# Optimization experiments

Measured on AMD Instinct MI355X. Metric: run time of the kernel, lower is better.

Reference implementation:

```python
import jax, jax.numpy as jnp
import numpy as np
from jax.scipy.special import logsumexp

N = 16    # taxa
K = 128   # particles
S = 512   # sites (batch == full sites)
A = 4     # alphabet (DNA)
D = 64    # embedding dim
C = 16    # site-position encoding dim
PRIOR_BL = 1.0
RATE = 1.0 / PRIOR_BL


def _log_double_factorials(n_max):
    v = np.zeros(n_max + 1)
    for i in range(2, n_max + 1):
        v[i] = v[i - 2] + np.log(i)
    return jnp.asarray(v, dtype=jnp.float32)

LOG_DF = _log_double_factorials(2 * N)


def _gather_K(arr, idx):
    return arr[jnp.arange(arr.shape[0]), idx]


def _remove2(arr_t, i1, i2):
    # drop entries i1, i2 along leading axis, preserving order (static output size t-2)
    t = arr_t.shape[0]
    ar = jnp.arange(t)
    keep = (ar != i1) & (ar != i2)
    order = jnp.argsort(~keep)[: t - 2]  # stable sort: kept entries first, in order
    return arr_t[order]


def _merge_K(arr, i1, i2, new_K):
    # replace_with_merged_K: remove the two merged subtrees, append the new one
    removed = jax.vmap(_remove2)(arr, i1, i2)
    return jnp.concatenate([removed, new_K[:, None]], axis=1)


def _stat_probs(emb_VxD, siteC_SxC, W_stat, W_site):
    logits = (emb_VxD @ W_stat)[:, None, :] + (siteC_SxC @ W_site)[None]  # V,S,A
    return jax.nn.softmax(logits, axis=-1)


def _log_P_F81(stat_KxSxA, b_K):
    # F81 rate matrix Q = pi - I  =>  P(t) = e^{-t} I + (1 - e^{-t}) pi (closed-form expm)
    e = jnp.exp(-b_K)[:, None, None, None]
    P = e * jnp.eye(A, dtype=stat_KxSxA.dtype) + (1.0 - e) * stat_KxSxA[:, :, None, :]
    return jnp.log(P + 1e-30)  # K,S,A,A


def _fel_half(logP, log_fel):
    # logsumexp_b ( logP[k,s,a,b] + log_fel[k,s,b] )
    return logsumexp(logP + log_fel[:, :, None, :], axis=-1)


def _forward(data_NxSxA, data_batched_NxSxA, site_positions_SxSfull, W_enc, W_merge, W_stat, W_pos, W_site):
    key = jax.random.key(42)
    siteC = site_positions_SxSfull @ W_pos                      # S,C
    emb0 = jnp.tanh(data_NxSxA.reshape(N, -1) @ W_enc)          # N,D (seq_encoder)
    embeddings = jnp.broadcast_to(emb0[None], (K, N, D))
    log_fel = jnp.broadcast_to(jnp.log(data_batched_NxSxA)[None], (K, N, S, A))
    leaf_counts = jnp.ones((K, N), jnp.int32)
    merge1 = jnp.zeros((K, 0), jnp.int32)
    merge2 = jnp.zeros((K, 0), jnp.int32)
    br1 = jnp.zeros((K, 0), dtype=data_NxSxA.dtype)
    br2 = jnp.zeros((K, 0), dtype=data_NxSxA.dtype)
    log_pi = jnp.zeros(K)
    log_w = jnp.zeros(K)
    log_lik = jnp.zeros(K)
    log_ws = []
    log_rate = jnp.log(jnp.asarray(RATE, data_NxSxA.dtype))
    for r in range(N - 1):
        t = N - r
        key, k1, k2, k3, k4 = jax.random.split(key, 5)
        # ---- categorical resampling ----
        idxK = jax.random.categorical(k1, log_w, shape=(K,))
        merge1, merge2 = merge1[idxK], merge2[idxK]
        br1, br2 = br1[idxK], br2[idxK]
        leaf_counts = leaf_counts[idxK]
        embeddings = embeddings[idxK]
        log_fel = log_fel[idxK]
        log_pi, log_w = log_pi[idxK], log_w[idxK]
        # ---- proposal: uniform pair + exponential branch lengths ----
        i1s, i2s = np.triu_indices(t, 1)
        npairs = len(i1s)
        p = jax.random.randint(k2, (K,), 0, npairs)
        idx1 = jnp.asarray(i1s, jnp.int32)[p]
        idx2 = jnp.asarray(i2s, jnp.int32)[p]
        b1 = jax.random.exponential(k3, (K,)) * PRIOR_BL
        b2 = jax.random.exponential(k4, (K,)) * PRIOR_BL
        log_v_plus = -jnp.log(float(npairs)) + (log_rate - RATE * b1) + (log_rate - RATE * b2)
        log_v_minus = jnp.zeros(K)
        e1, e2 = _gather_K(embeddings, idx1), _gather_K(embeddings, idx2)
        new_emb = jnp.tanh(jnp.concatenate([e1, e2], axis=-1) @ W_merge)  # K,D
        # ---- record merge history (concat_K) ----
        merge1 = jnp.concatenate([merge1, idx1[:, None]], axis=1)
        merge2 = jnp.concatenate([merge2, idx2[:, None]], axis=1)
        br1 = jnp.concatenate([br1, b1[:, None]], axis=1)
        br2 = jnp.concatenate([br2, b2[:, None]], axis=1)
        new_lc = _gather_K(leaf_counts, idx1) + _gather_K(leaf_counts, idx2)
        f1, f2 = _gather_K(log_fel, idx1), _gather_K(log_fel, idx2)
        leaf_counts = _merge_K(leaf_counts, idx1, idx2, new_lc)
        embeddings = _merge_K(embeddings, idx1, idx2, new_emb)
        # ---- Felsenstein pruning step at the new internal node ----
        stat_new = _stat_probs(new_emb, siteC, W_stat, W_site)  # K,S,A
        new_fel = _fel_half(_log_P_F81(stat_new, b1), f1) + _fel_half(_log_P_F81(stat_new, b2), f2)
        log_fel = _merge_K(log_fel, idx1, idx2, new_fel)
        # ---- forest log-likelihood and log pi ----
        tn = t - 1
        stat_all = _stat_probs(embeddings.reshape(K * tn, D), siteC, W_stat, W_site)
        log_stat = jnp.log(stat_all).reshape(K, tn, S, A)
        log_lik = jnp.sum(logsumexp(log_fel + log_stat, axis=-1), axis=(1, 2))  # K
        log_top = -jnp.sum(LOG_DF[jnp.clip(2 * leaf_counts - 3, 0)], axis=1)
        log_branch = jnp.sum(log_rate - RATE * br1, axis=1) + jnp.sum(log_rate - RATE * br2, axis=1)
        prev_log_pi = log_pi
        log_pi = log_lik + log_top + log_branch
        log_w = log_pi - prev_log_pi + log_v_minus - log_v_plus
        log_ws.append(log_w)
    log_ws = jnp.stack(log_ws)  # (N-1), K
    log_Z_SMC = jnp.sum(logsumexp(log_ws - jnp.log(float(K)), axis=1))
    best = jnp.argmax(log_lik)
    return (log_Z_SMC, log_lik, merge1[best], merge2[best], br1[best], br2[best])


def setup_inputs() -> dict:
    key = jax.random.key(0)
    ks = jax.random.split(key, 6)
    data = jax.random.uniform(ks[0], (N, S, A), minval=0.05, maxval=1.0)
    return {
        "data_NxSxA": data,
        "data_batched_NxSxA": data,
        "site_positions_SxSfull": jnp.eye(S, dtype=jnp.float32),
        "W_enc": jax.random.normal(ks[1], (S * A, D)) / float(np.sqrt(S * A)),
        "W_merge": jax.random.normal(ks[2], (2 * D, D)) / float(np.sqrt(2 * D)),
        "W_stat": jax.random.normal(ks[3], (D, A)) / float(np.sqrt(D)),
        "W_pos": jax.random.normal(ks[4], (S, C)) / float(np.sqrt(S)),
        "W_site": jax.random.normal(ks[5], (C, A)) / float(np.sqrt(C)),
    }


def reference(data_NxSxA, data_batched_NxSxA, site_positions_SxSfull, W_enc, W_merge, W_stat, W_pos, W_site):
    return _forward(data_NxSxA, data_batched_NxSxA, site_positions_SxSfull, W_enc, W_merge, W_stat, W_pos, W_site)
```

## Files before the change

kernel.cpp:

```cpp
#include <hip/hip_runtime.h>
#include <stdint.h>


#define NN 16
#define KK 128
#define SS 512
#define NR 15
#define PARTITIONABLE 1
#define TINYF 1.17549435e-38f
#define NROWS (NN + NR * KK)

__host__ __device__ __forceinline__ void tf2x32(uint32_t k0, uint32_t k1,
                                                uint32_t c0, uint32_t c1,
                                                uint32_t* o0, uint32_t* o1) {
  uint32_t ks2 = k0 ^ k1 ^ 0x1BD11BDAu;
  uint32_t x0 = c0 + k0, x1 = c1 + k1;
  uint32_t ks[3] = {k0, k1, ks2};
  const uint32_t RA[4] = {13u, 15u, 26u, 6u};
  const uint32_t RB[4] = {17u, 29u, 16u, 24u};
#pragma unroll
  for (int i = 0; i < 5; ++i) {
#pragma unroll
    for (int j = 0; j < 4; ++j) {
      uint32_t r = (i & 1) ? RB[j] : RA[j];
      x0 += x1;
      x1 = (x1 << r) | (x1 >> (32u - r));
      x1 ^= x0;
    }
    x0 += ks[(i + 1) % 3];
    x1 += ks[(i + 2) % 3] + (uint32_t)(i + 1);
  }
  *o0 = x0; *o1 = x1;
}

__device__ __forceinline__ uint32_t rbits32(uint32_t ka, uint32_t kb,
                                            uint32_t i, uint32_t total) {
#if PARTITIONABLE
  uint32_t o0, o1;
  tf2x32(ka, kb, 0u, i, &o0, &o1);
  return o0 ^ o1;
#else
  uint32_t half = total >> 1;
  uint32_t o0, o1;
  if (i < half) { tf2x32(ka, kb, i, i + half, &o0, &o1); return o0; }
  tf2x32(ka, kb, i - half, i, &o0, &o1);
  return o1;
#endif
}

__device__ __forceinline__ float bits_unif(uint32_t b) {
  return __uint_as_float((b >> 9) | 0x3f800000u) - 1.0f;
}

__device__ __forceinline__ float xla_tanh(float x) {
  float ax = fabsf(x);
  float xc = fminf(fmaxf(x, -7.90531110763549805f), 7.90531110763549805f);
  float x2 = __fmul_rn(xc, xc);
  float num = -2.76076847742355e-16f;
  num = __fadd_rn(__fmul_rn(x2, num), 2.00018790482477e-13f);
  num = __fadd_rn(__fmul_rn(x2, num), -8.60467152213735e-11f);
  num = __fadd_rn(__fmul_rn(x2, num), 5.12229709037114e-08f);
  num = __fadd_rn(__fmul_rn(x2, num), 1.48572235717979e-05f);
  num = __fadd_rn(__fmul_rn(x2, num), 6.37261928875436e-04f);
  num = __fadd_rn(__fmul_rn(x2, num), 4.89352455891786e-03f);
  num = __fmul_rn(xc, num);
  float den = 1.19825839466702e-06f;
  den = __fadd_rn(__fmul_rn(x2, den), 1.18534705686654e-04f);
  den = __fadd_rn(__fmul_rn(x2, den), 2.26843463243900e-03f);
  den = __fadd_rn(__fmul_rn(x2, den), 4.89352518554385e-03f);
  float r = __fdiv_rn(num, den);
  return (ax < 0.0004f) ? x : r;
}

__device__ __forceinline__ float fin_or0(float v) {
  return (v > -INFINITY && v < INFINITY) ? v : 0.0f;
}

__device__ __forceinline__ void fold8(float& ll, const float4* b4, int n4) {
  if (n4 <= 0) return;
  float4 pre[8];
#pragma unroll
  for (int i = 0; i < 8; ++i) pre[i] = b4[i];
  for (int q = 8; q <= n4; q += 8) {
    float4 cur[8];
#pragma unroll
    for (int i = 0; i < 8; ++i) cur[i] = pre[i];
    if (q < n4) {
#pragma unroll
      for (int i = 0; i < 8; ++i) pre[i] = b4[q + i];
    }
#pragma unroll
    for (int i = 0; i < 8; ++i) {
      ll = __fadd_rn(ll, cur[i].x);
      ll = __fadd_rn(ll, cur[i].y);
      ll = __fadd_rn(ll, cur[i].z);
      ll = __fadd_rn(ll, cur[i].w);
    }
  }
}

__global__ void k_setup(const float* datab, const float* Wpos, const float* Wsite,
                        float* fel_pool, float* sitelog, float* logw0,
                        float* logpi0, int* lc_pool, int* ilist0, float* logdf) {
  int b = blockIdx.x, tid = threadIdx.x;
  if (b < 64) {
    int id = b * 256 + tid;
    fel_pool[id] = logf(datab[id]);
    fel_pool[16384 + id] = logf(datab[16384 + id]);
  } else if (b < 72) {
    int id = (b - 64) * 256 + tid;
    int s = id >> 2, aa = id & 3;
    float acc = 0.0f;
    for (int c = 0; c < 16; ++c) acc = fmaf(Wpos[s * 16 + c], Wsite[c * 4 + aa], acc);
    sitelog[id] = acc;
  } else {
    if (tid < KK) {
      logw0[tid] = 0.0f;
      logpi0[tid] = 0.0f;
      for (int nn2 = 0; nn2 < NN; ++nn2) ilist0[tid * 16 + nn2] = nn2;
    }
    if (tid < NN) lc_pool[tid] = 1;
    if (tid == 0) {
      double vv[33];
      vv[0] = 0.0; vv[1] = 0.0;
      for (int i = 2; i <= 32; ++i) vv[i] = vv[i - 2] + log((double)i);
      for (int i = 0; i < 33; ++i) logdf[i] = (float)vv[i];
    }
  }
}

__global__ __launch_bounds__(64) void k_emb0(const float* data, const float* Wenc,
                                             const float* Wstat, float* emb_pool,
                                             float* ew0) {
  int n = blockIdx.x, d = threadIdx.x;
  __shared__ float ne[64];
  const float* dp = data + n * 2048;
  const float* wp = Wenc + d;
  float acc = 0.0f;
#pragma unroll 32
  for (int i = 0; i < 2048; ++i) acc = fmaf(dp[i], wp[(size_t)i * 64], acc);
  float v = xla_tanh(acc);
  ne[d] = v;
  emb_pool[n * 64 + d] = v;
  __syncthreads();
  if (d < 4) {
    float s = 0.0f;
    for (int c = 0; c < 64; ++c) s = fmaf(ne[c], Wstat[c * 4 + d], s);
    ew0[n * 4 + d] = s;
  }
}

__global__ void k_leafterm(const float* fel_pool, const float* ew0,
                           const float* sitelog, float* st_pool) {
  int id = blockIdx.x * blockDim.x + threadIdx.x;
  if (id >= NN * SS) return;
  int n = id >> 9, s = id & 511;
  float lg[4], ex[4], stat[4];
  for (int a = 0; a < 4; ++a) lg[a] = __fadd_rn(ew0[n * 4 + a], sitelog[s * 4 + a]);
  float m = lg[0];
  for (int a = 1; a < 4; ++a) m = fmaxf(m, lg[a]);
  float ssum = 0.0f;
  for (int a = 0; a < 4; ++a) { ex[a] = expf(__fsub_rn(lg[a], m)); ssum = __fadd_rn(ssum, ex[a]); }
  for (int a = 0; a < 4; ++a) stat[a] = __fdiv_rn(ex[a], ssum);
  float q[4], am = -INFINITY;
  for (int a = 0; a < 4; ++a) {
    q[a] = __fadd_rn(fel_pool[n * 2048 + s * 4 + a], logf(stat[a]));
    am = fmaxf(am, q[a]);
  }
  am = fin_or0(am);
  float se = 0.0f;
  for (int a = 0; a < 4; ++a) se = __fadd_rn(se, expf(__fsub_rn(q[a], am)));
  st_pool[n * 512 + s] = __fadd_rn(logf(se), am);
}

__global__ __launch_bounds__(256) void k_round(
    uint32_t ka, uint32_t kb, uint32_t k2a, uint32_t k2b,
    uint32_t k3a, uint32_t k3b, uint32_t k4a, uint32_t k4b,
    int t, int r,
    const float* logwC, float* logwN,
    const float* logpiC, float* logpiN,
    const int* ilistC, int* ilistN,
    const int* m1C, int* m1N, const int* m2C, int* m2N,
    const float* br1C, float* br1N, const float* br2C, float* br2N,
    float* emb_pool, float* fel_pool, float* st_pool, int* lc_pool,
    const float* Wmerge, const float* Wstat, const float* sitelog,
    const float* logdf, float* logws_r, float* loglik) {
  int k = blockIdx.x, tid = threadIdx.x;
  int tn = t - 1, tn2 = t - 2;
  int newrow = NN + r * KK + k;
  __shared__ float stbuf[15 * 512];
  __shared__ float cat[128];
  __shared__ float ne[64];
  __shared__ float ewl[4];
  __shared__ float smax[4];
  __shared__ int sidx[4];
  __shared__ int sI1, sI2;
  __shared__ float sB1, sB2, sLvp, sE1, sE2;
  __shared__ int ilN[16];
  __shared__ int lcb[16];
  __shared__ float brb1[15], brb2[15];

  float v = -INFINITY;
  if (tid < 128) {
    uint32_t bits = rbits32(ka, kb, (uint32_t)(k * KK + tid), KK * KK);
    float f = bits_unif(bits);
    float u = fmaxf(TINYF, __fadd_rn(f, TINYF));
    float gv = -logf(-logf(u));
    v = __fadd_rn(gv, logwC[tid]);
  } else if (tid == 128) {
    uint32_t h = rbits32(k2a, k2b, (uint32_t)k, 256u);
    uint32_t l = rbits32(k2a, k2b, (uint32_t)(128 + k), 256u);
    uint32_t span = (uint32_t)(t * (t - 1) / 2);
    uint32_t mult = 65536u % span;
    mult = (mult * mult) % span;
    uint32_t off = ((h % span) * mult + (l % span)) % span;
    int p = (int)off;
    int a1 = 0, rem = p, rl = t - 1;
    while (rem >= rl) { rem -= rl; ++a1; --rl; }
    sI1 = a1;
    sI2 = a1 + 1 + rem;
    uint32_t bb = rbits32(k3a, k3b, (uint32_t)k, 128u);
    float e1 = -log1pf(-bits_unif(bb));
    bb = rbits32(k4a, k4b, (uint32_t)k, 128u);
    float e2 = -log1pf(-bits_unif(bb));
    sB1 = e1; sB2 = e2;
    float lnp = logf((float)span);
    sLvp = __fadd_rn(__fadd_rn(-lnp, -e1), -e2);
  }
  float m = v;
  for (int d = 32; d > 0; d >>= 1) m = fmaxf(m, __shfl_xor(m, d, 64));
  int w = tid >> 6;
  if ((tid & 63) == 0) smax[w] = m;
  __syncthreads();
  float gm = fmaxf(fmaxf(smax[0], smax[1]), fmaxf(smax[2], smax[3]));
  int cand = (v == gm) ? tid : 9999;
  for (int d = 32; d > 0; d >>= 1) {
    int o = __shfl_xor(cand, d, 64);
    cand = (o < cand) ? o : cand;
  }
  if ((tid & 63) == 0) sidx[w] = cand;
  __syncthreads();
  int a;
  {
    int b0 = (sidx[0] < sidx[1]) ? sidx[0] : sidx[1];
    int b1_ = (sidx[2] < sidx[3]) ? sidx[2] : sidx[3];
    a = (b0 < b1_) ? b0 : b1_;
  }
  int i1 = sI1, i2 = sI2;
  int p1 = ilistC[a * 16 + i1];
  int p2 = ilistC[a * 16 + i2];

  if (tid < 64) {
    cat[tid] = emb_pool[p1 * 64 + tid];
    cat[64 + tid] = emb_pool[p2 * 64 + tid];
  } else if (tid >= 64 && tid < 80) {
    int pos = tid - 64;
    if (pos < tn2) {
      int src = pos + (pos >= i1) + (pos >= (i2 - 1));
      int row = ilistC[a * 16 + src];
      ilN[pos] = row;
      ilistN[k * 16 + pos] = row;
      lcb[pos] = lc_pool[row];
    } else if (pos == tn2) {
      ilN[pos] = newrow;
      ilistN[k * 16 + pos] = newrow;
      int lcnew = lc_pool[p1] + lc_pool[p2];
      lcb[pos] = lcnew;
      lc_pool[newrow] = lcnew;
    }
  } else if (tid >= 96 && tid < 96 + NR) {
    int j = tid - 96;
    if (j < r) {
      int v1 = m1C[a * 15 + j]; m1N[k * 15 + j] = v1;
      int v2 = m2C[a * 15 + j]; m2N[k * 15 + j] = v2;
      float w1 = br1C[a * 15 + j]; br1N[k * 15 + j] = w1; brb1[j] = w1;
      float w2 = br2C[a * 15 + j]; br2N[k * 15 + j] = w2; brb2[j] = w2;
    } else if (j == r) {
      m1N[k * 15 + r] = i1;
      m2N[k * 15 + r] = i2;
      br1N[k * 15 + r] = sB1;
      br2N[k * 15 + r] = sB2;
      brb1[r] = sB1;
      brb2[r] = sB2;
    }
  } else if (tid == 128) {
    sE1 = expf(-sB1);
  } else if (tid == 129) {
    sE2 = expf(-sB2);
  }
  __syncthreads();

  if (tid < 64) {
    float acc = 0.0f;
    for (int c = 0; c < 128; ++c) acc = fmaf(cat[c], Wmerge[c * 64 + tid], acc);
    float vv = xla_tanh(acc);
    ne[tid] = vv;
    emb_pool[newrow * 64 + tid] = vv;
  } else {
    int nf4 = tn2 * 128;
    int base = tid - 64;
    float4 tmp[10];
#pragma unroll
    for (int it = 0; it < 10; ++it) {
      int q = base + it * 192;
      if (q < nf4)
        tmp[it] = *(const float4*)(st_pool + (size_t)ilN[q >> 7] * 512 + ((q & 127) << 2));
    }
#pragma unroll
    for (int it = 0; it < 10; ++it) {
      int q = base + it * 192;
      if (q < nf4) ((float4*)stbuf)[q] = tmp[it];
    }
  }
  __syncthreads();

  if (tid < 4) {
    float s = 0.0f;
    for (int c = 0; c < 64; ++c) s = fmaf(ne[c], Wstat[c * 4 + tid], s);
    ewl[tid] = s;
  }
  __syncthreads();

  float ll = 0.0f;
  if (tid == 0) {
    fold8(ll, (const float4*)stbuf, tn2 * 128);
  } else if (tid >= 64) {
    float e1 = sE1, e2 = sE2;
    float om1 = __fsub_rn(1.0f, e1), om2 = __fsub_rn(1.0f, e2);
    float ewv[4];
#pragma unroll
    for (int aa = 0; aa < 4; ++aa) ewv[aa] = ewl[aa];
    for (int s = tid - 64; s < 512; s += 192) {
      float lg[4], ex[4], stat[4];
#pragma unroll
      for (int aa = 0; aa < 4; ++aa) lg[aa] = __fadd_rn(ewv[aa], sitelog[s * 4 + aa]);
      float mm = lg[0];
#pragma unroll
      for (int aa = 1; aa < 4; ++aa) mm = fmaxf(mm, lg[aa]);
      float ssum = 0.0f;
#pragma unroll
      for (int aa = 0; aa < 4; ++aa) {
        ex[aa] = expf(__fsub_rn(lg[aa], mm));
        ssum = __fadd_rn(ssum, ex[aa]);
      }
#pragma unroll
      for (int aa = 0; aa < 4; ++aa) stat[aa] = __fdiv_rn(ex[aa], ssum);
      float4 f1v = *(const float4*)(fel_pool + (size_t)p1 * 2048 + s * 4);
      float4 f2v = *(const float4*)(fel_pool + (size_t)p2 * 2048 + s * 4);
      float f1a[4] = {f1v.x, f1v.y, f1v.z, f1v.w};
      float f2a[4] = {f2v.x, f2v.y, f2v.z, f2v.w};
      float lo1[4], ld1[4], lo2[4], ld2[4];
#pragma unroll
      for (int bb = 0; bb < 4; ++bb) {
        float m1v = __fmul_rn(om1, stat[bb]);
        lo1[bb] = logf(__fadd_rn(m1v, 1e-30f));
        ld1[bb] = logf(__fadd_rn(__fadd_rn(e1, m1v), 1e-30f));
        float m2v = __fmul_rn(om2, stat[bb]);
        lo2[bb] = logf(__fadd_rn(m2v, 1e-30f));
        ld2[bb] = logf(__fadd_rn(__fadd_rn(e2, m2v), 1e-30f));
      }
      float nf[4];
#pragma unroll
      for (int aa = 0; aa < 4; ++aa) {
        float q1[4], am = -INFINITY;
#pragma unroll
        for (int bb = 0; bb < 4; ++bb) {
          q1[bb] = __fadd_rn((aa == bb) ? ld1[bb] : lo1[bb], f1a[bb]);
          am = fmaxf(am, q1[bb]);
        }
        am = fin_or0(am);
        float se = 0.0f;
#pragma unroll
        for (int bb = 0; bb < 4; ++bb) se = __fadd_rn(se, expf(__fsub_rn(q1[bb], am)));
        float h1 = __fadd_rn(logf(se), am);
        float q2[4], am2 = -INFINITY;
#pragma unroll
        for (int bb = 0; bb < 4; ++bb) {
          q2[bb] = __fadd_rn((aa == bb) ? ld2[bb] : lo2[bb], f2a[bb]);
          am2 = fmaxf(am2, q2[bb]);
        }
        am2 = fin_or0(am2);
        float se2 = 0.0f;
#pragma unroll
        for (int bb = 0; bb < 4; ++bb) se2 = __fadd_rn(se2, expf(__fsub_rn(q2[bb], am2)));
        float h2 = __fadd_rn(logf(se2), am2);
        nf[aa] = __fadd_rn(h1, h2);
      }
      *(float4*)(fel_pool + (size_t)newrow * 2048 + s * 4) =
          make_float4(nf[0], nf[1], nf[2], nf[3]);
      float q3[4], am3 = -INFINITY;
#pragma unroll
      for (int aa = 0; aa < 4; ++aa) {
        q3[aa] = __fadd_rn(nf[aa], logf(stat[aa]));
        am3 = fmaxf(am3, q3[aa]);
      }
      am3 = fin_or0(am3);
      float se3 = 0.0f;
#pragma unroll
      for (int aa = 0; aa < 4; ++aa) se3 = __fadd_rn(se3, expf(__fsub_rn(q3[aa], am3)));
      float stv = __fadd_rn(logf(se3), am3);
      stbuf[tn2 * 512 + s] = stv;
      st_pool[(size_t)newrow * 512 + s] = stv;
    }
  }
  __syncthreads();

  if (tid == 0) {
    fold8(ll, (const float4*)(stbuf + tn2 * 512), 128);
    float lt = 0.0f;
    for (int pos = 0; pos < tn; ++pos) {
      int idx = 2 * lcb[pos] - 3;
      if (idx < 0) idx = 0;
      lt = __fadd_rn(lt, logdf[idx]);
    }
    lt = -lt;
    float s1 = 0.0f, s2 = 0.0f;
    for (int j = 0; j <= r; ++j) {
      s1 = __fadd_rn(s1, -brb1[j]);
      s2 = __fadd_rn(s2, -brb2[j]);
    }
    float lb = __fadd_rn(s1, s2);
    float lpi = __fadd_rn(__fadd_rn(ll, lt), lb);
    float prev = logpiC[a];
    float lw = __fsub_rn(__fadd_rn(__fsub_rn(lpi, prev), 0.0f), sLvp);
    logpiN[k] = lpi;
    logwN[k] = lw;
    logws_r[k] = lw;
    loglik[k] = ll;
  }
}

__global__ void k_final(const float* logws, const float* loglik,
                        const int* m1D, const int* m2D,
                        const float* br1D, const float* br2D, float* out) {
  int j = threadIdx.x;
  out[1 + j] = loglik[j];
  __shared__ float sm[2];
  __shared__ float ssum[2];
  __shared__ int si[2];
  float c = logf(128.0f);
  float z = 0.0f;
  for (int r = 0; r < NR; ++r) {
    float v = __fsub_rn(logws[r * KK + j], c);
    float m = v;
    for (int d = 32; d > 0; d >>= 1) m = fmaxf(m, __shfl_xor(m, d, 64));
    if ((j & 63) == 0) sm[j >> 6] = m;
    __syncthreads();
    float gm = fin_or0(fmaxf(sm[0], sm[1]));
    float e = expf(__fsub_rn(v, gm));
    for (int d = 32; d > 0; d >>= 1) e = __fadd_rn(e, __shfl_xor(e, d, 64));
    if ((j & 63) == 0) ssum[j >> 6] = e;
    __syncthreads();
    if (j == 0) z = __fadd_rn(z, __fadd_rn(logf(__fadd_rn(ssum[0], ssum[1])), gm));
    __syncthreads();
  }
  if (j == 0) out[0] = z;
  float lv = loglik[j];
  float m2 = lv;
  for (int d = 32; d > 0; d >>= 1) m2 = fmaxf(m2, __shfl_xor(m2, d, 64));
  if ((j & 63) == 0) sm[j >> 6] = m2;
  __syncthreads();
  float gm2 = fmaxf(sm[0], sm[1]);
  int cand = (lv == gm2) ? j : 9999;
  for (int d = 32; d > 0; d >>= 1) {
    int o = __shfl_xor(cand, d, 64);
    cand = (o < cand) ? o : cand;
  }
  if ((j & 63) == 0) si[j >> 6] = cand;
  __syncthreads();
  int bi = (si[0] < si[1]) ? si[0] : si[1];
  if (j < NR) {
    out[129 + j] = (float)m1D[bi * 15 + j];
    out[144 + j] = (float)m2D[bi * 15 + j];
    out[159 + j] = br1D[bi * 15 + j];
    out[174 + j] = br2D[bi * 15 + j];
  }
}

static void split5_host(uint32_t* key0, uint32_t* key1, uint32_t out[8]) {
#if PARTITIONABLE
  uint32_t nk0, nk1, o0, o1;
  tf2x32(*key0, *key1, 0u, 0u, &nk0, &nk1);
  for (int j = 1; j < 5; ++j) {
    tf2x32(*key0, *key1, 0u, (uint32_t)j, &o0, &o1);
    out[2 * (j - 1)] = o0;
    out[2 * (j - 1) + 1] = o1;
  }
  *key0 = nk0; *key1 = nk1;
#else
  uint32_t a0[5], a1[5];
  for (int i = 0; i < 5; ++i) tf2x32(*key0, *key1, (uint32_t)i, (uint32_t)(i + 5), &a0[i], &a1[i]);
  uint32_t flat[10] = {a0[0], a0[1], a0[2], a0[3], a0[4], a1[0], a1[1], a1[2], a1[3], a1[4]};
  *key0 = flat[0]; *key1 = flat[1];
  for (int j = 0; j < 8; ++j) out[j] = flat[2 + j];
#endif
}

extern "C" void kernel_launch(void* const* d_in, const int* in_sizes, int n_in,
                              void* d_out, int out_size, void* d_ws, size_t ws_size,
                              hipStream_t stream) {
  const float* data = (const float*)d_in[0];
  const float* datab = (const float*)d_in[1];
  const float* Wenc = (const float*)d_in[3];
  const float* Wmerge = (const float*)d_in[4];
  const float* Wstat = (const float*)d_in[5];
  const float* Wpos = (const float*)d_in[6];
  const float* Wsite = (const float*)d_in[7];
  float* out = (float*)d_out;

  char* base = (char*)d_ws;
  size_t off = 0;
  auto alloc = [&](size_t bytes) -> void* {
    void* p = base + off;
    off += (bytes + 255) & ~(size_t)255;
    return p;
  };
  float* fel_pool = (float*)alloc((size_t)NROWS * 2048 * 4);
  float* st_pool = (float*)alloc((size_t)NROWS * 512 * 4);
  float* emb_pool = (float*)alloc((size_t)NROWS * 64 * 4);
  int* lc_pool = (int*)alloc((size_t)NROWS * 4);
  int* ilist[2]; int* m1[2]; int* m2[2]; float* br1[2]; float* br2[2];
  float* logpi[2]; float* logw2[2];
  for (int b = 0; b < 2; ++b) ilist[b] = (int*)alloc((size_t)KK * 16 * 4);
  for (int b = 0; b < 2; ++b) m1[b] = (int*)alloc((size_t)KK * 15 * 4);
  for (int b = 0; b < 2; ++b) m2[b] = (int*)alloc((size_t)KK * 15 * 4);
  for (int b = 0; b < 2; ++b) br1[b] = (float*)alloc((size_t)KK * 15 * 4);
  for (int b = 0; b < 2; ++b) br2[b] = (float*)alloc((size_t)KK * 15 * 4);
  for (int b = 0; b < 2; ++b) logpi[b] = (float*)alloc((size_t)KK * 4);
  for (int b = 0; b < 2; ++b) logw2[b] = (float*)alloc((size_t)KK * 4);
  float* logws = (float*)alloc(NR * KK * 4);
  float* loglik = (float*)alloc(KK * 4);
  float* sitelog = (float*)alloc(SS * 4 * 4);
  float* logdf = (float*)alloc(33 * 4);
  float* ew0 = (float*)alloc(NN * 4 * 4);
  (void)ws_size; (void)in_sizes; (void)n_in; (void)out_size;

  k_setup<<<73, 256, 0, stream>>>(datab, Wpos, Wsite, fel_pool, sitelog,
                                  logw2[0], logpi[0], lc_pool, ilist[0], logdf);
  k_emb0<<<NN, 64, 0, stream>>>(data, Wenc, Wstat, emb_pool, ew0);
  k_leafterm<<<32, 256, 0, stream>>>(fel_pool, ew0, sitelog, st_pool);

  uint32_t key0 = 0u, key1 = 42u;
  for (int r = 0; r < NR; ++r) {
    uint32_t ks[8];
    split5_host(&key0, &key1, ks);
    int t = NN - r;
    int cur = r & 1, nxt = cur ^ 1;
    k_round<<<KK, 256, 0, stream>>>(
        ks[0], ks[1], ks[2], ks[3], ks[4], ks[5], ks[6], ks[7], t, r,
        logw2[cur], logw2[nxt], logpi[cur], logpi[nxt],
        ilist[cur], ilist[nxt], m1[cur], m1[nxt], m2[cur], m2[nxt],
        br1[cur], br1[nxt], br2[cur], br2[nxt],
        emb_pool, fel_pool, st_pool, lc_pool,
        Wmerge, Wstat, sitelog, logdf, logws + r * KK, loglik);
  }
  k_final<<<1, 128, 0, stream>>>(logws, loglik, m1[1], m2[1], br1[1], br2[1], out);
}
```

Before: 504.2 us.

## Fuse setup and all SMC rounds into one persistent kernel with grid barriers

Replaces the setup, embedding, leaf-term and fifteen per-round kernel launches with one persistent kernel of 128 blocks. Blocks synchronise between stages through an atomic-counter grid barrier. This removes repeated launch overhead and inter-kernel gaps on the stream. It relies on all 128 blocks being co-resident, and the spin barrier adds atomic polling latency at each round.

Result: slower. 648.5 us (+28.6%).

```diff
diff --git a/kernel.cpp b/kernel.cpp
--- a/kernel.cpp
+++ b/kernel.cpp
@@ -1,5 +1,6 @@
 #include <hip/hip_runtime.h>
 #include <stdint.h>
+#include <string.h>
 
 
 #define NN 16
@@ -99,95 +100,32 @@
   }
 }
 
-__global__ void k_setup(const float* datab, const float* Wpos, const float* Wsite,
-                        float* fel_pool, float* sitelog, float* logw0,
-                        float* logpi0, int* lc_pool, int* ilist0, float* logdf) {
-  int b = blockIdx.x, tid = threadIdx.x;
-  if (b < 64) {
-    int id = b * 256 + tid;
-    fel_pool[id] = logf(datab[id]);
-    fel_pool[16384 + id] = logf(datab[16384 + id]);
-  } else if (b < 72) {
-    int id = (b - 64) * 256 + tid;
-    int s = id >> 2, aa = id & 3;
-    float acc = 0.0f;
-    for (int c = 0; c < 16; ++c) acc = fmaf(Wpos[s * 16 + c], Wsite[c * 4 + aa], acc);
-    sitelog[id] = acc;
-  } else {
-    if (tid < KK) {
-      logw0[tid] = 0.0f;
-      logpi0[tid] = 0.0f;
-      for (int nn2 = 0; nn2 < NN; ++nn2) ilist0[tid * 16 + nn2] = nn2;
-    }
-    if (tid < NN) lc_pool[tid] = 1;
-    if (tid == 0) {
-      double vv[33];
-      vv[0] = 0.0; vv[1] = 0.0;
-      for (int i = 2; i <= 32; ++i) vv[i] = vv[i - 2] + log((double)i);
-      for (int i = 0; i < 33; ++i) logdf[i] = (float)vv[i];
-    }
-  }
-}
-
-__global__ __launch_bounds__(64) void k_emb0(const float* data, const float* Wenc,
-                                             const float* Wstat, float* emb_pool,
-                                             float* ew0) {
-  int n = blockIdx.x, d = threadIdx.x;
-  __shared__ float ne[64];
-  const float* dp = data + n * 2048;
-  const float* wp = Wenc + d;
-  float acc = 0.0f;
-#pragma unroll 32
-  for (int i = 0; i < 2048; ++i) acc = fmaf(dp[i], wp[(size_t)i * 64], acc);
-  float v = xla_tanh(acc);
-  ne[d] = v;
-  emb_pool[n * 64 + d] = v;
+__device__ __forceinline__ void gbar(unsigned* ctr, unsigned phase) {
   __syncthreads();
-  if (d < 4) {
-    float s = 0.0f;
-    for (int c = 0; c < 64; ++c) s = fmaf(ne[c], Wstat[c * 4 + d], s);
-    ew0[n * 4 + d] = s;
-  }
-}
-
-__global__ void k_leafterm(const float* fel_pool, const float* ew0,
-                           const float* sitelog, float* st_pool) {
-  int id = blockIdx.x * blockDim.x + threadIdx.x;
-  if (id >= NN * SS) return;
-  int n = id >> 9, s = id & 511;
-  float lg[4], ex[4], stat[4];
-  for (int a = 0; a < 4; ++a) lg[a] = __fadd_rn(ew0[n * 4 + a], sitelog[s * 4 + a]);
-  float m = lg[0];
-  for (int a = 1; a < 4; ++a) m = fmaxf(m, lg[a]);
-  float ssum = 0.0f;
-  for (int a = 0; a < 4; ++a) { ex[a] = expf(__fsub_rn(lg[a], m)); ssum = __fadd_rn(ssum, ex[a]); }
-  for (int a = 0; a < 4; ++a) stat[a] = __fdiv_rn(ex[a], ssum);
-  float q[4], am = -INFINITY;
-  for (int a = 0; a < 4; ++a) {
-    q[a] = __fadd_rn(fel_pool[n * 2048 + s * 4 + a], logf(stat[a]));
-    am = fmaxf(am, q[a]);
-  }
-  am = fin_or0(am);
-  float se = 0.0f;
-  for (int a = 0; a < 4; ++a) se = __fadd_rn(se, expf(__fsub_rn(q[a], am)));
-  st_pool[n * 512 + s] = __fadd_rn(logf(se), am);
-}
-
-__global__ __launch_bounds__(256) void k_round(
-    uint32_t ka, uint32_t kb, uint32_t k2a, uint32_t k2b,
-    uint32_t k3a, uint32_t k3b, uint32_t k4a, uint32_t k4b,
-    int t, int r,
-    const float* logwC, float* logwN,
-    const float* logpiC, float* logpiN,
-    const int* ilistC, int* ilistN,
-    const int* m1C, int* m1N, const int* m2C, int* m2N,
-    const float* br1C, float* br1N, const float* br2C, float* br2N,
-    float* emb_pool, float* fel_pool, float* st_pool, int* lc_pool,
-    const float* Wmerge, const float* Wstat, const float* sitelog,
-    const float* logdf, float* logws_r, float* loglik) {
-  int k = blockIdx.x, tid = threadIdx.x;
-  int tn = t - 1, tn2 = t - 2;
-  int newrow = NN + r * KK + k;
+  if (threadIdx.x == 0) {
+    __threadfence();
+    atomicAdd(ctr, 1u);
+    unsigned target = 128u * phase;
+    while (atomicAdd(ctr, 0u) < target) { __builtin_amdgcn_s_sleep(2); }
+    __threadfence();
+  }
+  __syncthreads();
+}
+
+struct KeysAll { uint32_t v[NR][8]; };
+
+__global__ __launch_bounds__(256) void k_mega(
+    KeysAll keys,
+    const float* data, const float* datab,
+    const float* Wenc, const float* Wmerge, const float* Wstat,
+    const float* Wpos, const float* Wsite,
+    float* fel_pool, float* st_pool, float* emb_pool, int* lc_pool,
+    int* ilist0, int* ilist1, int* m1_0, int* m1_1, int* m2_0, int* m2_1,
+    float* br1_0, float* br1_1, float* br2_0, float* br2_1,
+    float* logpi_0, float* logpi_1, float* logw_0, float* logw_1,
+    float* logws, float* loglik, float* sitelog, float* logdf, float* ew0,
+    unsigned* ctr) {
+  int blk = blockIdx.x, tid = threadIdx.x;
   __shared__ float stbuf[15 * 512];
   __shared__ float cat[128];
   __shared__ float ne[64];
@@ -200,233 +138,324 @@
   __shared__ int lcb[16];
   __shared__ float brb1[15], brb2[15];
 
-  float v = -INFINITY;
-  if (tid < 128) {
-    uint32_t bits = rbits32(ka, kb, (uint32_t)(k * KK + tid), KK * KK);
-    float f = bits_unif(bits);
-    float u = fmaxf(TINYF, __fadd_rn(f, TINYF));
-    float gv = -logf(-logf(u));
-    v = __fadd_rn(gv, logwC[tid]);
-  } else if (tid == 128) {
-    uint32_t h = rbits32(k2a, k2b, (uint32_t)k, 256u);
-    uint32_t l = rbits32(k2a, k2b, (uint32_t)(128 + k), 256u);
-    uint32_t span = (uint32_t)(t * (t - 1) / 2);
-    uint32_t mult = 65536u % span;
-    mult = (mult * mult) % span;
-    uint32_t off = ((h % span) * mult + (l % span)) % span;
-    int p = (int)off;
-    int a1 = 0, rem = p, rl = t - 1;
-    while (rem >= rl) { rem -= rl; ++a1; --rl; }
-    sI1 = a1;
-    sI2 = a1 + 1 + rem;
-    uint32_t bb = rbits32(k3a, k3b, (uint32_t)k, 128u);
-    float e1 = -log1pf(-bits_unif(bb));
-    bb = rbits32(k4a, k4b, (uint32_t)k, 128u);
-    float e2 = -log1pf(-bits_unif(bb));
-    sB1 = e1; sB2 = e2;
-    float lnp = logf((float)span);
-    sLvp = __fadd_rn(__fadd_rn(-lnp, -e1), -e2);
-  }
-  float m = v;
-  for (int d = 32; d > 0; d >>= 1) m = fmaxf(m, __shfl_xor(m, d, 64));
-  int w = tid >> 6;
-  if ((tid & 63) == 0) smax[w] = m;
-  __syncthreads();
-  float gm = fmaxf(fmaxf(smax[0], smax[1]), fmaxf(smax[2], smax[3]));
-  int cand = (v == gm) ? tid : 9999;
-  for (int d = 32; d > 0; d >>= 1) {
-    int o = __shfl_xor(cand, d, 64);
-    cand = (o < cand) ? o : cand;
-  }
-  if ((tid & 63) == 0) sidx[w] = cand;
-  __syncthreads();
-  int a;
-  {
-    int b0 = (sidx[0] < sidx[1]) ? sidx[0] : sidx[1];
-    int b1_ = (sidx[2] < sidx[3]) ? sidx[2] : sidx[3];
-    a = (b0 < b1_) ? b0 : b1_;
-  }
-  int i1 = sI1, i2 = sI2;
-  int p1 = ilistC[a * 16 + i1];
-  int p2 = ilistC[a * 16 + i2];
+  { int id = blk * 256 + tid; fel_pool[id] = logf(datab[id]); }
+  if (blk < 8) {
+    int id = blk * 256 + tid;
+    int s = id >> 2, aa = id & 3;
+    float acc = 0.0f;
+    for (int c = 0; c < 16; ++c) acc = fmaf(Wpos[s * 16 + c], Wsite[c * 4 + aa], acc);
+    sitelog[id] = acc;
+  }
+  if (blk == 16) {
+    if (tid < KK) {
+      logw_0[tid] = 0.0f;
+      logpi_0[tid] = 0.0f;
+      for (int n = 0; n < NN; ++n) ilist0[tid * 16 + n] = n;
+    }
+    if (tid < NN) lc_pool[tid] = 1;
+    if (tid == 0) {
+      double vv[33];
+      vv[0] = 0.0; vv[1] = 0.0;
+      for (int i = 2; i <= 32; ++i) vv[i] = vv[i - 2] + log((double)i);
+      for (int i = 0; i < 33; ++i) logdf[i] = (float)vv[i];
+    }
+  }
+  if (blk < 16) {
+    if (tid < 64) {
+      const float* dp = data + blk * 2048;
+      const float* wp = Wenc + tid;
+      float acc = 0.0f;
+#pragma unroll 32
+      for (int i = 0; i < 2048; ++i) acc = fmaf(dp[i], wp[(size_t)i * 64], acc);
+      float v = xla_tanh(acc);
+      ne[tid] = v;
+      emb_pool[blk * 64 + tid] = v;
+    }
+    __syncthreads();
+    if (tid < 4) {
+      float s = 0.0f;
+      for (int c = 0; c < 64; ++c) s = fmaf(ne[c], Wstat[c * 4 + tid], s);
+      ew0[blk * 4 + tid] = s;
+    }
+  }
+  gbar(ctr, 1);
 
   if (tid < 64) {
-    cat[tid] = emb_pool[p1 * 64 + tid];
-    cat[64 + tid] = emb_pool[p2 * 64 + tid];
-  } else if (tid >= 64 && tid < 80) {
-    int pos = tid - 64;
-    if (pos < tn2) {
-      int src = pos + (pos >= i1) + (pos >= (i2 - 1));
-      int row = ilistC[a * 16 + src];
-      ilN[pos] = row;
-      ilistN[k * 16 + pos] = row;
-      lcb[pos] = lc_pool[row];
-    } else if (pos == tn2) {
-      ilN[pos] = newrow;
-      ilistN[k * 16 + pos] = newrow;
-      int lcnew = lc_pool[p1] + lc_pool[p2];
-      lcb[pos] = lcnew;
-      lc_pool[newrow] = lcnew;
-    }
-  } else if (tid >= 96 && tid < 96 + NR) {
-    int j = tid - 96;
-    if (j < r) {
-      int v1 = m1C[a * 15 + j]; m1N[k * 15 + j] = v1;
-      int v2 = m2C[a * 15 + j]; m2N[k * 15 + j] = v2;
-      float w1 = br1C[a * 15 + j]; br1N[k * 15 + j] = w1; brb1[j] = w1;
-      float w2 = br2C[a * 15 + j]; br2N[k * 15 + j] = w2; brb2[j] = w2;
-    } else if (j == r) {
-      m1N[k * 15 + r] = i1;
-      m2N[k * 15 + r] = i2;
-      br1N[k * 15 + r] = sB1;
-      br2N[k * 15 + r] = sB2;
-      brb1[r] = sB1;
-      brb2[r] = sB2;
-    }
-  } else if (tid == 128) {
-    sE1 = expf(-sB1);
-  } else if (tid == 129) {
-    sE2 = expf(-sB2);
-  }
-  __syncthreads();
-
-  if (tid < 64) {
-    float acc = 0.0f;
-    for (int c = 0; c < 128; ++c) acc = fmaf(cat[c], Wmerge[c * 64 + tid], acc);
-    float vv = xla_tanh(acc);
-    ne[tid] = vv;
-    emb_pool[newrow * 64 + tid] = vv;
-  } else {
-    int nf4 = tn2 * 128;
-    int base = tid - 64;
-    float4 tmp[10];
-#pragma unroll
-    for (int it = 0; it < 10; ++it) {
-      int q = base + it * 192;
-      if (q < nf4)
-        tmp[it] = *(const float4*)(st_pool + (size_t)ilN[q >> 7] * 512 + ((q & 127) << 2));
-    }
-#pragma unroll
-    for (int it = 0; it < 10; ++it) {
-      int q = base + it * 192;
-      if (q < nf4) ((float4*)stbuf)[q] = tmp[it];
-    }
-  }
-  __syncthreads();
-
-  if (tid < 4) {
-    float s = 0.0f;
-    for (int c = 0; c < 64; ++c) s = fmaf(ne[c], Wstat[c * 4 + tid], s);
-    ewl[tid] = s;
-  }
-  __syncthreads();
-
-  float ll = 0.0f;
-  if (tid == 0) {
-    fold8(ll, (const float4*)stbuf, tn2 * 128);
-  } else if (tid >= 64) {
-    float e1 = sE1, e2 = sE2;
-    float om1 = __fsub_rn(1.0f, e1), om2 = __fsub_rn(1.0f, e2);
-    float ewv[4];
-#pragma unroll
-    for (int aa = 0; aa < 4; ++aa) ewv[aa] = ewl[aa];
-    for (int s = tid - 64; s < 512; s += 192) {
-      float lg[4], ex[4], stat[4];
-#pragma unroll
-      for (int aa = 0; aa < 4; ++aa) lg[aa] = __fadd_rn(ewv[aa], sitelog[s * 4 + aa]);
-      float mm = lg[0];
-#pragma unroll
-      for (int aa = 1; aa < 4; ++aa) mm = fmaxf(mm, lg[aa]);
-      float ssum = 0.0f;
-#pragma unroll
-      for (int aa = 0; aa < 4; ++aa) {
-        ex[aa] = expf(__fsub_rn(lg[aa], mm));
-        ssum = __fadd_rn(ssum, ex[aa]);
-      }
-#pragma unroll
-      for (int aa = 0; aa < 4; ++aa) stat[aa] = __fdiv_rn(ex[aa], ssum);
-      float4 f1v = *(const float4*)(fel_pool + (size_t)p1 * 2048 + s * 4);
-      float4 f2v = *(const float4*)(fel_pool + (size_t)p2 * 2048 + s * 4);
-      float f1a[4] = {f1v.x, f1v.y, f1v.z, f1v.w};
-      float f2a[4] = {f2v.x, f2v.y, f2v.z, f2v.w};
-      float lo1[4], ld1[4], lo2[4], ld2[4];
-#pragma unroll
-      for (int bb = 0; bb < 4; ++bb) {
-        float m1v = __fmul_rn(om1, stat[bb]);
-        lo1[bb] = logf(__fadd_rn(m1v, 1e-30f));
-        ld1[bb] = logf(__fadd_rn(__fadd_rn(e1, m1v), 1e-30f));
-        float m2v = __fmul_rn(om2, stat[bb]);
-        lo2[bb] = logf(__fadd_rn(m2v, 1e-30f));
-        ld2[bb] = logf(__fadd_rn(__fadd_rn(e2, m2v), 1e-30f));
-      }
-      float nf[4];
-#pragma unroll
-      for (int aa = 0; aa < 4; ++aa) {
-        float q1[4], am = -INFINITY;
+    int id = blk * 64 + tid;
+    int n = id >> 9, s = id & 511;
+    float lg[4], ex[4], stat[4];
+    for (int a = 0; a < 4; ++a) lg[a] = __fadd_rn(ew0[n * 4 + a], sitelog[s * 4 + a]);
+    float m = lg[0];
+    for (int a = 1; a < 4; ++a) m = fmaxf(m, lg[a]);
+    float ssum = 0.0f;
+    for (int a = 0; a < 4; ++a) { ex[a] = expf(__fsub_rn(lg[a], m)); ssum = __fadd_rn(ssum, ex[a]); }
+    for (int a = 0; a < 4; ++a) stat[a] = __fdiv_rn(ex[a], ssum);
+    float q[4], am = -INFINITY;
+    for (int a = 0; a < 4; ++a) {
+      q[a] = __fadd_rn(fel_pool[n * 2048 + s * 4 + a], logf(stat[a]));
+      am = fmaxf(am, q[a]);
+    }
+    am = fin_or0(am);
+    float se = 0.0f;
+    for (int a = 0; a < 4; ++a) se = __fadd_rn(se, expf(__fsub_rn(q[a], am)));
+    st_pool[n * 512 + s] = __fadd_rn(logf(se), am);
+  }
+  gbar(ctr, 2);
+
+  int k = blk;
+  for (int r = 0; r < NR; ++r) {
+    int t = NN - r;
+    int tn = t - 1, tn2 = t - 2;
+    int newrow = NN + r * KK + k;
+    int cur = r & 1;
+    const float* logwC = cur ? logw_1 : logw_0;
+    float* logwN = cur ? logw_0 : logw_1;
+    const float* logpiC = cur ? logpi_1 : logpi_0;
+    float* logpiN = cur ? logpi_0 : logpi_1;
+    const int* ilistC = cur ? ilist1 : ilist0;
+    int* ilistN = cur ? ilist0 : ilist1;
+    const int* m1C = cur ? m1_1 : m1_0;
+    int* m1N = cur ? m1_0 : m1_1;
+    const int* m2C = cur ? m2_1 : m2_0;
+    int* m2N = cur ? m2_0 : m2_1;
+    const float* br1C = cur ? br1_1 : br1_0;
+    float* br1N = cur ? br1_0 : br1_1;
+    const float* br2C = cur ? br2_1 : br2_0;
+    float* br2N = cur ? br2_0 : br2_1;
+    uint32_t ka = keys.v[r][0], kb = keys.v[r][1];
+    uint32_t k2a = keys.v[r][2], k2b = keys.v[r][3];
+    uint32_t k3a = keys.v[r][4], k3b = keys.v[r][5];
+    uint32_t k4a = keys.v[r][6], k4b = keys.v[r][7];
+
+    float v = -INFINITY;
+    if (tid < 128) {
+      uint32_t bits = rbits32(ka, kb, (uint32_t)(k * KK + tid), KK * KK);
+      float f = bits_unif(bits);
+      float u = fmaxf(TINYF, __fadd_rn(f, TINYF));
+      float gv = -logf(-logf(u));
+      v = __fadd_rn(gv, logwC[tid]);
+    } else if (tid == 128) {
+      uint32_t h = rbits32(k2a, k2b, (uint32_t)k, 256u);
+      uint32_t l = rbits32(k2a, k2b, (uint32_t)(128 + k), 256u);
+      uint32_t span = (uint32_t)(t * (t - 1) / 2);
+      uint32_t mult = 65536u % span;
+      mult = (mult * mult) % span;
+      uint32_t off = ((h % span) * mult + (l % span)) % span;
+      int p = (int)off;
+      int a1 = 0, rem = p, rl = t - 1;
+      while (rem >= rl) { rem -= rl; ++a1; --rl; }
+      sI1 = a1;
+      sI2 = a1 + 1 + rem;
+      uint32_t bb = rbits32(k3a, k3b, (uint32_t)k, 128u);
+      float e1 = -log1pf(-bits_unif(bb));
+      bb = rbits32(k4a, k4b, (uint32_t)k, 128u);
+      float e2 = -log1pf(-bits_unif(bb));
+      sB1 = e1; sB2 = e2;
+      float lnp = logf((float)span);
+      sLvp = __fadd_rn(__fadd_rn(-lnp, -e1), -e2);
+    }
+    float m = v;
+    for (int d = 32; d > 0; d >>= 1) m = fmaxf(m, __shfl_xor(m, d, 64));
+    int w = tid >> 6;
+    if ((tid & 63) == 0) smax[w] = m;
+    __syncthreads();
+    float gm = fmaxf(fmaxf(smax[0], smax[1]), fmaxf(smax[2], smax[3]));
+    int cand = (v == gm) ? tid : 9999;
+    for (int d = 32; d > 0; d >>= 1) {
+      int o = __shfl_xor(cand, d, 64);
+      cand = (o < cand) ? o : cand;
+    }
+    if ((tid & 63) == 0) sidx[w] = cand;
+    __syncthreads();
+    int a;
+    {
+      int b0 = (sidx[0] < sidx[1]) ? sidx[0] : sidx[1];
+      int b1_ = (sidx[2] < sidx[3]) ? sidx[2] : sidx[3];
+      a = (b0 < b1_) ? b0 : b1_;
+    }
+    int i1 = sI1, i2 = sI2;
+    int p1 = ilistC[a * 16 + i1];
+    int p2 = ilistC[a * 16 + i2];
+
+    if (tid < 64) {
+      cat[tid] = emb_pool[p1 * 64 + tid];
+      cat[64 + tid] = emb_pool[p2 * 64 + tid];
+    } else if (tid >= 64 && tid < 80) {
+      int pos = tid - 64;
+      if (pos < tn2) {
+        int src = pos + (pos >= i1) + (pos >= (i2 - 1));
+        int row = ilistC[a * 16 + src];
+        ilN[pos] = row;
+        ilistN[k * 16 + pos] = row;
+        lcb[pos] = lc_pool[row];
+      } else if (pos == tn2) {
+        ilN[pos] = newrow;
+        ilistN[k * 16 + pos] = newrow;
+        int lcnew = lc_pool[p1] + lc_pool[p2];
+        lcb[pos] = lcnew;
+        lc_pool[newrow] = lcnew;
+      }
+    } else if (tid >= 96 && tid < 96 + NR) {
+      int j = tid - 96;
+      if (j < r) {
+        int v1 = m1C[a * 15 + j]; m1N[k * 15 + j] = v1;
+        int v2 = m2C[a * 15 + j]; m2N[k * 15 + j] = v2;
+        float w1 = br1C[a * 15 + j]; br1N[k * 15 + j] = w1; brb1[j] = w1;
+        float w2 = br2C[a * 15 + j]; br2N[k * 15 + j] = w2; brb2[j] = w2;
+      } else if (j == r) {
+        m1N[k * 15 + r] = i1;
+        m2N[k * 15 + r] = i2;
+        br1N[k * 15 + r] = sB1;
+        br2N[k * 15 + r] = sB2;
+        brb1[r] = sB1;
+        brb2[r] = sB2;
+      }
+    } else if (tid == 128) {
+      sE1 = expf(-sB1);
+    } else if (tid == 129) {
+      sE2 = expf(-sB2);
+    }
+    __syncthreads();
+
+    if (tid < 64) {
+      float acc = 0.0f;
+      for (int c = 0; c < 128; ++c) acc = fmaf(cat[c], Wmerge[c * 64 + tid], acc);
+      float vv = xla_tanh(acc);
+      ne[tid] = vv;
+      emb_pool[newrow * 64 + tid] = vv;
+    } else {
+      int nf4 = tn2 * 128;
+      int base = tid - 64;
+      float4 tmp[10];
+#pragma unroll
+      for (int it = 0; it < 10; ++it) {
+        int q = base + it * 192;
+        if (q < nf4)
+          tmp[it] = *(const float4*)(st_pool + (size_t)ilN[q >> 7] * 512 + ((q & 127) << 2));
+      }
+#pragma unroll
+      for (int it = 0; it < 10; ++it) {
+        int q = base + it * 192;
+        if (q < nf4) ((float4*)stbuf)[q] = tmp[it];
+      }
+    }
+    __syncthreads();
+
+    if (tid < 4) {
+      float s = 0.0f;
+      for (int c = 0; c < 64; ++c) s = fmaf(ne[c], Wstat[c * 4 + tid], s);
+      ewl[tid] = s;
+    }
+    __syncthreads();
+
+    float ll = 0.0f;
+    if (tid == 0) {
+      fold8(ll, (const float4*)stbuf, tn2 * 128);
+    } else if (tid >= 64) {
+      float e1 = sE1, e2 = sE2;
+      float om1 = __fsub_rn(1.0f, e1), om2 = __fsub_rn(1.0f, e2);
+      float ewv[4];
+#pragma unroll
+      for (int aa = 0; aa < 4; ++aa) ewv[aa] = ewl[aa];
+      for (int s = tid - 64; s < 512; s += 192) {
+        float lg[4], ex[4], stat[4];
+#pragma unroll
+        for (int aa = 0; aa < 4; ++aa) lg[aa] = __fadd_rn(ewv[aa], sitelog[s * 4 + aa]);
+        float mm = lg[0];
+#pragma unroll
+        for (int aa = 1; aa < 4; ++aa) mm = fmaxf(mm, lg[aa]);
+        float ssum = 0.0f;
+#pragma unroll
+        for (int aa = 0; aa < 4; ++aa) {
+          ex[aa] = expf(__fsub_rn(lg[aa], mm));
+          ssum = __fadd_rn(ssum, ex[aa]);
+        }
+#pragma unroll
+        for (int aa = 0; aa < 4; ++aa) stat[aa] = __fdiv_rn(ex[aa], ssum);
+        float4 f1v = *(const float4*)(fel_pool + (size_t)p1 * 2048 + s * 4);
+        float4 f2v = *(const float4*)(fel_pool + (size_t)p2 * 2048 + s * 4);
+        float f1a[4] = {f1v.x, f1v.y, f1v.z, f1v.w};
+        float f2a[4] = {f2v.x, f2v.y, f2v.z, f2v.w};
+        float lo1[4], ld1[4], lo2[4], ld2[4];
 #pragma unroll
         for (int bb = 0; bb < 4; ++bb) {
-          q1[bb] = __fadd_rn((aa == bb) ? ld1[bb] : lo1[bb], f1a[bb]);
-          am = fmaxf(am, q1[bb]);
+          float m1v = __fmul_rn(om1, stat[bb]);
+          lo1[bb] = logf(__fadd_rn(m1v, 1e-30f));
+          ld1[bb] = logf(__fadd_rn(__fadd_rn(e1, m1v), 1e-30f));
+          float m2v = __fmul_rn(om2, stat[bb]);
+          lo2[bb] = logf(__fadd_rn(m2v, 1e-30f));
+          ld2[bb] = logf(__fadd_rn(__fadd_rn(e2, m2v), 1e-30f));
         }
-        am = fin_or0(am);
-        float se = 0.0f;
-#pragma unroll
-        for (int bb = 0; bb < 4; ++bb) se = __fadd_rn(se, expf(__fsub_rn(q1[bb], am)));
-        float h1 = __fadd_rn(logf(se), am);
-        float q2[4], am2 = -INFINITY;
-#pragma unroll
-        for (int bb = 0; bb < 4; ++bb) {
-          q2[bb] = __fadd_rn((aa == bb) ? ld2[bb] : lo2[bb], f2a[bb]);
-          am2 = fmaxf(am2, q2[bb]);
+        float nf[4];
+#pragma unroll
+        for (int aa = 0; aa < 4; ++aa) {
+          float q1[4], am = -INFINITY;
+#pragma unroll
+          for (int bb = 0; bb < 4; ++bb) {
+            q1[bb] = __fadd_rn((aa == bb) ? ld1[bb] : lo1[bb], f1a[bb]);
+            am = fmaxf(am, q1[bb]);
+          }
+          am = fin_or0(am);
+          float se = 0.0f;
+#pragma unroll
+          for (int bb = 0; bb < 4; ++bb) se = __fadd_rn(se, expf(__fsub_rn(q1[bb], am)));
+          float h1 = __fadd_rn(logf(se), am);
+          float q2[4], am2 = -INFINITY;
+#pragma unroll
+          for (int bb = 0; bb < 4; ++bb) {
+            q2[bb] = __fadd_rn((aa == bb) ? ld2[bb] : lo2[bb], f2a[bb]);
+            am2 = fmaxf(am2, q2[bb]);
+          }
+          am2 = fin_or0(am2);
+          float se2 = 0.0f;
+#pragma unroll
+          for (int bb = 0; bb < 4; ++bb) se2 = __fadd_rn(se2, expf(__fsub_rn(q2[bb], am2)));
+          float h2 = __fadd_rn(logf(se2), am2);
+          nf[aa] = __fadd_rn(h1, h2);
         }
-        am2 = fin_or0(am2);
-        float se2 = 0.0f;
-#pragma unroll
-        for (int bb = 0; bb < 4; ++bb) se2 = __fadd_rn(se2, expf(__fsub_rn(q2[bb], am2)));
-        float h2 = __fadd_rn(logf(se2), am2);
-        nf[aa] = __fadd_rn(h1, h2);
-      }
-      *(float4*)(fel_pool + (size_t)newrow * 2048 + s * 4) =
-          make_float4(nf[0], nf[1], nf[2], nf[3]);
-      float q3[4], am3 = -INFINITY;
-#pragma unroll
-      for (int aa = 0; aa < 4; ++aa) {
-        q3[aa] = __fadd_rn(nf[aa], logf(stat[aa]));
-        am3 = fmaxf(am3, q3[aa]);
-      }
-      am3 = fin_or0(am3);
-      float se3 = 0.0f;
-#pragma unroll
-      for (int aa = 0; aa < 4; ++aa) se3 = __fadd_rn(se3, expf(__fsub_rn(q3[aa], am3)));
-      float stv = __fadd_rn(logf(se3), am3);
-      stbuf[tn2 * 512 + s] = stv;
-      st_pool[(size_t)newrow * 512 + s] = stv;
-    }
-  }
-  __syncthreads();
-
-  if (tid == 0) {
-    fold8(ll, (const float4*)(stbuf + tn2 * 512), 128);
-    float lt = 0.0f;
-    for (int pos = 0; pos < tn; ++pos) {
-      int idx = 2 * lcb[pos] - 3;
-      if (idx < 0) idx = 0;
-      lt = __fadd_rn(lt, logdf[idx]);
-    }
-    lt = -lt;
-    float s1 = 0.0f, s2 = 0.0f;
-    for (int j = 0; j <= r; ++j) {
-      s1 = __fadd_rn(s1, -brb1[j]);
-      s2 = __fadd_rn(s2, -brb2[j]);
-    }
-    float lb = __fadd_rn(s1, s2);
-    float lpi = __fadd_rn(__fadd_rn(ll, lt), lb);
-    float prev = logpiC[a];
-    float lw = __fsub_rn(__fadd_rn(__fsub_rn(lpi, prev), 0.0f), sLvp);
-    logpiN[k] = lpi;
-    logwN[k] = lw;
-    logws_r[k] = lw;
-    loglik[k] = ll;
+        *(float4*)(fel_pool + (size_t)newrow * 2048 + s * 4) =
+            make_float4(nf[0], nf[1], nf[2], nf[3]);
+        float q3[4], am3 = -INFINITY;
+#pragma unroll
+        for (int aa = 0; aa < 4; ++aa) {
+          q3[aa] = __fadd_rn(nf[aa], logf(stat[aa]));
+          am3 = fmaxf(am3, q3[aa]);
+        }
+        am3 = fin_or0(am3);
+        float se3 = 0.0f;
+#pragma unroll
+        for (int aa = 0; aa < 4; ++aa) se3 = __fadd_rn(se3, expf(__fsub_rn(q3[aa], am3)));
+        float stv = __fadd_rn(logf(se3), am3);
+        stbuf[tn2 * 512 + s] = stv;
+        st_pool[(size_t)newrow * 512 + s] = stv;
+      }
+    }
+    __syncthreads();
+
+    if (tid == 0) {
+      fold8(ll, (const float4*)(stbuf + tn2 * 512), 128);
+      float lt = 0.0f;
+      for (int pos = 0; pos < tn; ++pos) {
+        int idx = 2 * lcb[pos] - 3;
+        if (idx < 0) idx = 0;
+        lt = __fadd_rn(lt, logdf[idx]);
+      }
+      lt = -lt;
+      float s1 = 0.0f, s2 = 0.0f;
+      for (int j = 0; j <= r; ++j) {
+        s1 = __fadd_rn(s1, -brb1[j]);
+        s2 = __fadd_rn(s2, -brb2[j]);
+      }
+      float lb = __fadd_rn(s1, s2);
+      float lpi = __fadd_rn(__fadd_rn(ll, lt), lb);
+      float prev = logpiC[a];
+      float lw = __fsub_rn(__fadd_rn(__fsub_rn(lpi, prev), 0.0f), sLvp);
+      logpiN[k] = lpi;
+      logwN[k] = lw;
+      logws[r * KK + k] = lw;
+      loglik[k] = ll;
+    }
+    gbar(ctr, 3u + (unsigned)r);
   }
 }
 
@@ -533,26 +562,20 @@
   float* sitelog = (float*)alloc(SS * 4 * 4);
   float* logdf = (float*)alloc(33 * 4);
   float* ew0 = (float*)alloc(NN * 4 * 4);
+  unsigned* ctr = (unsigned*)alloc(256);
   (void)ws_size; (void)in_sizes; (void)n_in; (void)out_size;
 
-  k_setup<<<73, 256, 0, stream>>>(datab, Wpos, Wsite, fel_pool, sitelog,
-                                  logw2[0], logpi[0], lc_pool, ilist[0], logdf);
-  k_emb0<<<NN, 64, 0, stream>>>(data, Wenc, Wstat, emb_pool, ew0);
-  k_leafterm<<<32, 256, 0, stream>>>(fel_pool, ew0, sitelog, st_pool);
-
+  KeysAll keys;
   uint32_t key0 = 0u, key1 = 42u;
-  for (int r = 0; r < NR; ++r) {
-    uint32_t ks[8];
-    split5_host(&key0, &key1, ks);
-    int t = NN - r;
-    int cur = r & 1, nxt = cur ^ 1;
-    k_round<<<KK, 256, 0, stream>>>(
-        ks[0], ks[1], ks[2], ks[3], ks[4], ks[5], ks[6], ks[7], t, r,
-        logw2[cur], logw2[nxt], logpi[cur], logpi[nxt],
-        ilist[cur], ilist[nxt], m1[cur], m1[nxt], m2[cur], m2[nxt],
-        br1[cur], br1[nxt], br2[cur], br2[nxt],
-        emb_pool, fel_pool, st_pool, lc_pool,
-        Wmerge, Wstat, sitelog, logdf, logws + r * KK, loglik);
-  }
+  for (int r = 0; r < NR; ++r) split5_host(&key0, &key1, keys.v[r]);
+
+  hipMemsetAsync(ctr, 0, sizeof(unsigned), stream);
+  k_mega<<<KK, 256, 0, stream>>>(
+      keys, data, datab, Wenc, Wmerge, Wstat, Wpos, Wsite,
+      fel_pool, st_pool, emb_pool, lc_pool,
+      ilist[0], ilist[1], m1[0], m1[1], m2[0], m2[1],
+      br1[0], br1[1], br2[0], br2[1],
+      logpi[0], logpi[1], logw2[0], logw2[1],
+      logws, loglik, sitelog, logdf, ew0, ctr);
   k_final<<<1, 128, 0, stream>>>(logws, loglik, m1[1], m2[1], br1[1], br2[1], out);
 }
```
